# Kernel tuning notes

Hardware: AMD Instinct MI355X
Metric: run time of the kernel (lower is better)

The kernel has to match this reference:

```python
import jax, jax.numpy as jnp
import numpy as np

B, HH, WW, C, HEADS = 2, 128, 128, 256, 8
D = C // HEADS


def setup_inputs() -> dict:
    key = jax.random.key(0)
    ks = jax.random.split(key, 24)
    def nrm(k, shape, s=0.02):
        return jax.random.normal(k, shape, jnp.float32) * s
    inp = {
        'x_2': jax.random.normal(ks[0], (B, HH, WW, C), jnp.float32),
        'x_4': jax.random.normal(ks[1], (B, HH, WW, C), jnp.float32),
        'x_8': jax.random.normal(ks[2], (B, HH, WW, C), jnp.float32),
        'y':   jax.random.normal(ks[3], (B, HH, WW, C), jnp.float32),
        'Wqm': nrm(ks[4], (C, C)), 'Wkm': nrm(ks[5], (C, C)), 'Wvm': nrm(ks[6], (C, C)),
        'Wk2': nrm(ks[7], (C, C)), 'Wv2': nrm(ks[8], (C, C)),
        'Wk4': nrm(ks[9], (C, C)), 'Wv4': nrm(ks[10], (C, C)),
        'Wk8': nrm(ks[11], (C, C)), 'Wv8': nrm(ks[12], (C, C)),
        'rescalem': jnp.ones((HEADS, 1, 1), jnp.float32),
        'rescale2': jnp.ones((HEADS, 1, 1), jnp.float32),
        'rescale4': jnp.ones((HEADS, 1, 1), jnp.float32),
        'rescale8': jnp.ones((HEADS, 1, 1), jnp.float32),
        'Wproj': nrm(ks[13], (C, C)), 'bproj': jnp.zeros((C,), jnp.float32),
        'Wpos1': nrm(ks[14], (C, 1, 3, 3)), 'Wpos2': nrm(ks[15], (C, 1, 3, 3)),
    }
    return inp


def _l2norm(x):
    # F.normalize(p=2, dim=-1): x / max(||x||_2, eps)
    return x / jnp.maximum(jnp.linalg.norm(x, axis=-1, keepdims=True), 1e-12)


def _heads_T(t):
    # (b, n, h*d) -> (b, h, d, n)  (split heads then transpose last two dims)
    b, n, _ = t.shape
    return t.reshape(b, n, HEADS, D).transpose(0, 2, 3, 1)


def _dwconv(x, w):
    # x: NCHW, w: (C,1,3,3) depthwise
    return jax.lax.conv_general_dilated(
        x, w, (1, 1), 'SAME',
        dimension_numbers=('NCHW', 'OIHW', 'NCHW'),
        feature_group_count=C)


def reference(x_2, x_4, x_8, y,
              Wqm, Wkm, Wvm, Wk2, Wv2, Wk4, Wv4, Wk8, Wv8,
              rescalem, rescale2, rescale4, rescale8,
              Wproj, bproj, Wpos1, Wpos2):
    b, h, w, c = y.shape
    n = h * w
    x2 = x_2.reshape(b, n, c)
    x4 = x_4.reshape(b, n, c)
    x8 = x_8.reshape(b, n, c)
    yf = y.reshape(b, n, c)

    q_inpm = yf @ Wqm.T
    v_inpm = yf @ Wvm.T
    qm = _l2norm(_heads_T(q_inpm))  # (b,heads,d,n), L2-normalized over n

    def branch(k_inp, v_inp, rescale):
        k = _l2norm(_heads_T(k_inp))   # (b,heads,d,n)
        v = _heads_T(v_inp)            # (b,heads,d,n)
        attn = jnp.einsum('bhdn,bhen->bhde', k, qm) * rescale  # (b,heads,d,d)
        attn = jax.nn.softmax(attn, axis=-1)
        return jnp.einsum('bhde,bhen->bhdn', attn, v)

    # NOTE: original code uses rescale4 for the x8 branch (faithful to source).
    xo = (branch(yf @ Wkm.T, v_inpm, rescalem)
          + branch(x2 @ Wk2.T, x2 @ Wv2.T, rescale2)
          + branch(x4 @ Wk4.T, x4 @ Wv4.T, rescale4)
          + branch(x8 @ Wk8.T, x8 @ Wv8.T, rescale4))

    # (b,heads,d,n) -> (b,n,heads*d)
    xo = xo.transpose(0, 3, 1, 2).reshape(b, n, HEADS * D)
    out_c = (xo @ Wproj.T + bproj).reshape(b, h, w, c)

    p = v_inpm.reshape(b, h, w, c).transpose(0, 3, 1, 2)  # NCHW
    p = _dwconv(p, Wpos1)
    p = jax.nn.gelu(p, approximate=False)
    p = _dwconv(p, Wpos2)
    out_p = p.transpose(0, 2, 3, 1)

    return out_c + out_p
```

## Files before the change

kernel.cpp:

```cpp
#include <hip/hip_runtime.h>
#include <hip/hip_bf16.h>
#include <math.h>

typedef short bf16x8 __attribute__((ext_vector_type(8)));
typedef float f32x4 __attribute__((ext_vector_type(4)));

#define MFMA16(a,b,c) __builtin_amdgcn_mfma_f32_16x16x32_bf16(a,b,c,0,0,0)

__device__ inline short f2bf(float f){
  union{ __hip_bfloat16 h; short s; } u;
  u.h = __float2bfloat16(f);
  return u.s;
}
__device__ inline float bf2f(short s){
  uint32_t u = ((uint32_t)(uint16_t)s) << 16;
  return __builtin_bit_cast(float, u);
}
__device__ inline void store8bf(short* dst, float4 a, float4 b){
  union{ short s[8]; int4 q; } u;
  u.s[0]=f2bf(a.x); u.s[1]=f2bf(a.y); u.s[2]=f2bf(a.z); u.s[3]=f2bf(a.w);
  u.s[4]=f2bf(b.x); u.s[5]=f2bf(b.y); u.s[6]=f2bf(b.z); u.s[7]=f2bf(b.w);
  *(int4*)dst = u.q;
}

__device__ inline void gld16(const void* g, void* l){
  __builtin_amdgcn_global_load_lds(
      (const __attribute__((address_space(1))) unsigned int*)g,
      (__attribute__((address_space(3))) unsigned int*)l, 16, 0, 0);
}

#define BARC() do{ asm volatile("":::"memory"); __builtin_amdgcn_s_barrier(); \
                   asm volatile("":::"memory"); }while(0)

__global__ __launch_bounds__(256) void k_cvt(const float* __restrict__ src, short* __restrict__ dst, int n){
  int i = blockIdx.x*256 + threadIdx.x;
  if(i < n) dst[i] = f2bf(src[i]);
}

__global__ __launch_bounds__(256) void k_cvtN(const float* __restrict__ src, short* __restrict__ dst,
                                              int n, int ncpy){
  int i = blockIdx.x*256 + threadIdx.x;
  if(i >= n) return;
  float s = src[i];
  for(int c=1;c<ncpy;++c) s += src[i + (size_t)c*917504];
  dst[i] = f2bf(s);
}

__global__ __launch_bounds__(256) void k_wvt(const float* __restrict__ wm, const float* __restrict__ w2,
                                             const float* __restrict__ w4, const float* __restrict__ w8,
                                             short* __restrict__ wvT){
  int t = blockIdx.x*256 + threadIdx.x;
  int br = t >> 16; int rem = t & 65535; int a = rem >> 8, j = rem & 255;
  const float* w = (br==0)? wm : (br==1)? w2 : (br==2)? w4 : w8;
  wvT[t] = f2bf(w[j*256 + a]);
}

__global__ __launch_bounds__(256) void k_wT(const float* __restrict__ w1, const float* __restrict__ w2,
                                            float* __restrict__ wT){
  int t = blockIdx.x*256 + threadIdx.x;
  if(t >= 4608) return;
  int cv = t / 2304; int rem = t % 2304; int tap = rem >> 8; int c = rem & 255;
  const float* w = cv ? w2 : w1;
  wT[t] = w[c*9 + tap];
}

__global__ __launch_bounds__(256) void k_pack(const float* __restrict__ x2, const float* __restrict__ x4,
                                              const float* __restrict__ x8, const float* __restrict__ y,
                                              short* __restrict__ xt){
  int sb = blockIdx.z; int s = sb >> 1, b = sb & 1;
  const float* src = ((s==0)? y : (s==1)? x2 : (s==2)? x4 : x8) + (size_t)b*16384*256;
  __shared__ short tile[64*264];
  int t = threadIdx.x, l = t & 63, w = t >> 6;
  int n0 = blockIdx.x*64;
  #pragma unroll
  for(int p=0;p<16;++p){
    int row = p*4 + w;
    float4 v = *(const float4*)(src + (size_t)(n0+row)*256 + 4*l);
    union{ short s4[4]; int2 q; } u;
    u.s4[0]=f2bf(v.x); u.s4[1]=f2bf(v.y); u.s4[2]=f2bf(v.z); u.s4[3]=f2bf(v.w);
    *(int2*)&tile[row*264 + 4*l] = u.q;
  }
  __syncthreads();
  int c = t;
  short* outb = xt + ((size_t)sb*512 + (n0>>5))*8192;
  int sw = (c>>1)&3;
  #pragma unroll
  for(int ti=0; ti<2; ++ti){
    union{ short v[32]; int4 q4[4]; } rowv;
    #pragma unroll
    for(int j=0;j<32;++j) rowv.v[j] = tile[(ti*32+j)*264 + c];
    char* ob = (char*)(outb + (size_t)ti*8192 + c*32);
    #pragma unroll
    for(int hi=0;hi<4;++hi)
      *(int4*)(ob + ((hi ^ sw)<<4)) = rowv.q4[hi];
  }
}

__device__ inline bf16x8 tfrag(const short* base, int c, int hi){
  int byte = c*64 + ((hi ^ ((c>>1)&3))<<4);
  return *(const bf16x8*)((const char*)base + byte);
}

__global__ __launch_bounds__(512,2) void k_cov(const short* __restrict__ xt, float* __restrict__ covF,
                                               int plain){
  int jb = blockIdx.x;
  int ck = blockIdx.y;
  int j = jb >> 1, b = jb & 1;
  int t = threadIdx.x, l = t & 63, w = t >> 6;
  int lr = l & 15, hi = l >> 4;
  __shared__ short lds3[3][16384];
  int su = (j < 4) ? 0 : (j - 3);
  int sv = (j == 0) ? 0 : ((j < 4) ? j : (j - 3));
  int sym = (su == sv);
  const short* Ug = xt + (size_t)(su*2+b)*512*8192;
  const short* Vg = xt + (size_t)(sv*2+b)*512*8192;
  int nt0 = ck*32;

  f32x4 acc[2][16];
  #pragma unroll
  for(int i=0;i<2;++i)
    #pragma unroll
    for(int n2=0;n2<16;++n2) acc[i][n2] = (f32x4){0.f,0.f,0.f,0.f};

  #define STAGE_S(bufi, kk) do{                                                 \
    const short* Ut_ = Ug + (size_t)(nt0+(kk))*8192;                            \
    short* dst_ = &lds3[bufi][0];                                               \
    _Pragma("unroll")                                                           \
    for(int i_=0;i_<2;++i_){ int ch_ = w*2+i_;                                  \
      gld16(Ut_ + ch_*512 + l*8, dst_ + ch_*512); }                             \
  }while(0)
  #define STAGE_A(bufi, kk) do{                                                 \
    const short* Ut_ = Ug + (size_t)(nt0+(kk))*8192;                            \
    const short* Vt_ = Vg + (size_t)(nt0+(kk))*8192;                            \
    short* dst_ = &lds3[bufi][0];                                               \
    _Pragma("unroll")                                                           \
    for(int i_=0;i_<4;++i_){ int ch_ = w*4+i_;                                  \
      const short* g_ = (ch_<16) ? (Ut_ + ch_*512 + l*8)                        \
                                 : (Vt_ + (ch_-16)*512 + l*8);                  \
      gld16(g_, dst_ + ch_*512); }                                              \
  }while(0)
  #define COMPUTE(bufp, vofs) do{                                               \
    const short* Ub_ = bufp;                                                    \
    const short* Vb_ = Ub_ + (vofs);                                            \
    bf16x8 a0_ = tfrag(Ub_, w*32 + lr, hi);                                     \
    bf16x8 a1_ = tfrag(Ub_, w*32 + 16 + lr, hi);                                \
    _Pragma("unroll")                                                           \
    for(int nt_=0;nt_<16;++nt_){                                                \
      bf16x8 bb_ = tfrag(Vb_, nt_*16 + lr, hi);                                 \
      acc[0][nt_] = MFMA16(a0_, bb_, acc[0][nt_]);                              \
      acc[1][nt_] = MFMA16(a1_, bb_, acc[1][nt_]);                              \
    }                                                                           \
  }while(0)

  if(sym){
    STAGE_S(0,0); STAGE_S(1,1); STAGE_S(2,2);
    asm volatile("s_waitcnt vmcnt(4)":::"memory");
    BARC();
    int buf = 0;
    #pragma unroll 1
    for(int k=0;k<32;++k){
      COMPUTE(&lds3[buf][0], 0);
      if(k==31) break;
      BARC();
      if(k < 29){
        STAGE_S(buf, k+3);
        asm volatile("s_waitcnt vmcnt(4)":::"memory");
      } else if(k == 29){
        asm volatile("s_waitcnt vmcnt(2)":::"memory");
      } else {
        asm volatile("s_waitcnt vmcnt(0)":::"memory");
      }
      BARC();
      buf = (buf==2)?0:(buf+1);
    }
  } else {
    STAGE_A(0,0); STAGE_A(1,1); STAGE_A(2,2);
    asm volatile("s_waitcnt vmcnt(8)":::"memory");
    BARC();
    int buf = 0;
    #pragma unroll 1
    for(int k=0;k<32;++k){
      COMPUTE(&lds3[buf][0], 8192);
      if(k==31) break;
      BARC();
      if(k < 29){
        STAGE_A(buf, k+3);
        asm volatile("s_waitcnt vmcnt(8)":::"memory");
      } else if(k == 29){
        asm volatile("s_waitcnt vmcnt(4)":::"memory");
      } else {
        asm volatile("s_waitcnt vmcnt(0)":::"memory");
      }
      BARC();
      buf = (buf==2)?0:(buf+1);
    }
  }
  #undef STAGE_S
  #undef STAGE_A
  #undef COMPUTE

  if(plain){
    float* cov = covF + (size_t)ck*917504 + (size_t)jb*65536;
    #pragma unroll
    for(int rt=0;rt<2;++rt)
      #pragma unroll
      for(int nt=0;nt<16;++nt)
        #pragma unroll
        for(int r=0;r<4;++r){
          int row = w*32 + rt*16 + 4*hi + r;
          int col = nt*16 + lr;
          cov[(size_t)row*256 + col] = acc[rt][nt][r];
        }
  } else {
    float* cov = covF + (size_t)jb*65536;
    #pragma unroll
    for(int rt=0;rt<2;++rt)
      #pragma unroll
      for(int nt=0;nt<16;++nt)
        #pragma unroll
        for(int r=0;r<4;++r){
          int row = w*32 + rt*16 + 4*hi + r;
          int col = nt*16 + lr;
          atomicAdd(&cov[(size_t)row*256 + col], acc[rt][nt][r]);
        }
  }
}

__device__ inline void mm_32x256(const short (*wA)[264], const short* __restrict__ covbf,
                                 short (*tmp)[264], int t){
  int l = t & 63, w = t >> 6;
  int mt = w >> 1, ntb = (w & 1)*8;
  f32x4 acc[8];
  #pragma unroll
  for(int i=0;i<8;++i) acc[i] = (f32x4){0.f,0.f,0.f,0.f};
  #pragma unroll
  for(int kk=0; kk<8; ++kk){
    bf16x8 a = *(const bf16x8*)&wA[16*mt + (l&15)][kk*32 + 8*(l>>4)];
    #pragma unroll
    for(int n=0; n<8; ++n){
      int j = (ntb+n)*16 + (l&15);
      bf16x8 bb = *(const bf16x8*)&covbf[(size_t)j*256 + kk*32 + 8*(l>>4)];
      acc[n] = MFMA16(a, bb, acc[n]);
    }
  }
  #pragma unroll
  for(int n=0;n<8;++n)
    #pragma unroll
    for(int r=0;r<4;++r)
      tmp[16*mt + 4*(l>>4) + r][(ntb+n)*16 + (l&15)] = f2bf(acc[n][r]);
}
__device__ inline void mm_32x32(const short (*A)[264], const short (*Bw)[264], float (*M)[33], int t){
  int l = t & 63, w = t >> 6;
  int mt = w >> 1, nt = w & 1;
  f32x4 acc = (f32x4){0.f,0.f,0.f,0.f};
  #pragma unroll
  for(int kk=0; kk<8; ++kk){
    bf16x8 a = *(const bf16x8*)&A[16*mt + (l&15)][kk*32 + 8*(l>>4)];
    bf16x8 b = *(const bf16x8*)&Bw[16*nt + (l&15)][kk*32 + 8*(l>>4)];
    acc = MFMA16(a, b, acc);
  }
  #pragma unroll
  for(int r=0;r<4;++r)
    M[16*mt + 4*(l>>4) + r][16*nt + (l&15)] = acc[r];
}

__global__ __launch_bounds__(256) void k_attn(
    const float* __restrict__ Wq, const float* __restrict__ Wkm, const float* __restrict__ Wk2,
    const float* __restrict__ Wk4, const float* __restrict__ Wk8,
    const float* __restrict__ rsm, const float* __restrict__ rs2, const float* __restrict__ rs4,
    const short* __restrict__ covB, float* __restrict__ Aout){
  int h = blockIdx.x, b = blockIdx.y, br = blockIdx.z;
  int t = threadIdx.x;
  __shared__ short wk[32][264], wq[32][264], tmp[32][264];
  __shared__ float Ml[32][33];
  __shared__ float nrm[64];
  const float* Wk = (br==0)? Wkm : (br==1)? Wk2 : (br==2)? Wk4 : Wk8;
  {
    int d = t >> 3, c0 = (t & 7)*32;
    const float* pk = Wk + (size_t)(h*32+d)*256 + c0;
    const float* pq = Wq + (size_t)(h*32+d)*256 + c0;
    #pragma unroll
    for(int i=0;i<32;i+=8){
      float4 a1 = *(const float4*)(pk+i), a2 = *(const float4*)(pk+i+4);
      store8bf(&wk[d][c0+i], a1, a2);
      float4 b1 = *(const float4*)(pq+i), b2 = *(const float4*)(pq+i+4);
      store8bf(&wq[d][c0+i], b1, b2);
    }
  }
  __syncthreads();
  const short* cxy = covB + (size_t)(br*2+b)*65536;
  const short* cxx = (br==0)? cxy : covB + (size_t)(8 + (br-1)*2 + b)*65536;
  const short* cyy = covB + (size_t)b*65536;
  mm_32x256(wk, cxx, tmp, t); __syncthreads();
  mm_32x32(tmp, wk, Ml, t);   __syncthreads();
  if(t < 32) nrm[t] = Ml[t][t];
  __syncthreads();
  mm_32x256(wq, cyy, tmp, t); __syncthreads();
  mm_32x32(tmp, wq, Ml, t);   __syncthreads();
  if(t < 32) nrm[32+t] = Ml[t][t];
  __syncthreads();
  mm_32x256(wk, cxy, tmp, t); __syncthreads();
  mm_32x32(tmp, wq, Ml, t);   __syncthreads();
  if(t < 32){
    int d = t;
    const float* rs = (br==0)? rsm : (br==1)? rs2 : rs4;
    float rsv = rs[h];
    float invk = 1.f / fmaxf(sqrtf(fmaxf(nrm[d], 0.f)), 1e-12f);
    float lg[32]; float mx = -1e30f;
    #pragma unroll
    for(int e=0;e<32;++e){
      float invq = 1.f / fmaxf(sqrtf(fmaxf(nrm[32+e], 0.f)), 1e-12f);
      float v = Ml[d][e] * invk * invq * rsv;
      lg[e] = v; mx = fmaxf(mx, v);
    }
    float sum = 0.f;
    #pragma unroll
    for(int e=0;e<32;++e){ lg[e] = expf(lg[e]-mx); sum += lg[e]; }
    float inv = 1.f/sum;
    float* Ao = Aout + ((size_t)((br*2+b)*8 + h))*1024 + d*32;
    #pragma unroll
    for(int e=0;e<32;++e) Ao[e] = lg[e]*inv;
  }
}

__global__ __launch_bounds__(256) void k_qfold(const float* __restrict__ Wproj, const float* __restrict__ Ain,
                                               const short* __restrict__ wvT, short* __restrict__ qf){
  int cg = blockIdx.x, b = blockIdx.y, br = blockIdx.z;
  int t = threadIdx.x;
  __shared__ float Al[8*1036];
  __shared__ short pl[32][264];
  const float* Ag = Ain + (size_t)((br*2+b)*8)*1024;
  for(int i=t; i<8192; i+=256){
    int hh = i >> 10, dd = (i >> 5) & 31, ee = i & 31;
    Al[hh*1036 + dd*32 + ee] = Ag[i];
  }
  __syncthreads();
  {
    int c = cg*32 + (t >> 3), h = t & 7;
    const float* wpr = Wproj + (size_t)c*256 + h*32;
    float wp[32];
    #pragma unroll
    for(int i=0;i<32;i+=4){
      float4 v = *(const float4*)(wpr+i);
      wp[i]=v.x; wp[i+1]=v.y; wp[i+2]=v.z; wp[i+3]=v.w;
    }
    float pv[32];
    #pragma unroll
    for(int e=0;e<32;++e) pv[e]=0.f;
    const float* Ah = Al + h*1036;
    #pragma unroll
    for(int d=0; d<32; ++d){
      float wpd = wp[d];
      #pragma unroll
      for(int e=0;e<32;e+=4){
        float4 av = *(const float4*)&Ah[d*32+e];
        pv[e]   += wpd*av.x; pv[e+1] += wpd*av.y;
        pv[e+2] += wpd*av.z; pv[e+3] += wpd*av.w;
      }
    }
    #pragma unroll
    for(int e=0;e<32;++e) pl[t>>3][h*32+e] = f2bf(pv[e]);
  }
  __syncthreads();
  {
    int l = t & 63, w = t >> 6, mt = w >> 1, ntb = (w & 1)*8;
    const short* wvt = wvT + (size_t)br*65536;
    f32x4 acc[8];
    #pragma unroll
    for(int i=0;i<8;++i) acc[i] = (f32x4){0.f,0.f,0.f,0.f};
    #pragma unroll
    for(int kk=0; kk<8; ++kk){
      bf16x8 a = *(const bf16x8*)&pl[16*mt + (l&15)][kk*32 + 8*(l>>4)];
      #pragma unroll
      for(int n=0;n<8;++n){
        int arow = (ntb+n)*16 + (l&15);
        bf16x8 bb = *(const bf16x8*)&wvt[(size_t)arow*256 + kk*32 + 8*(l>>4)];
        acc[n] = MFMA16(a, bb, acc[n]);
      }
    }
    short* qfp = qf + (size_t)(br*2+b)*65536;
    #pragma unroll
    for(int n=0;n<8;++n)
      #pragma unroll
      for(int r=0;r<4;++r){
        int row = cg*32 + 16*mt + 4*(l>>4) + r;
        int col = (ntb+n)*16 + (l&15);
        qfp[(size_t)row*256 + col] = f2bf(acc[n][r]);
      }
  }
}

__device__ inline void at_write4(short* base, int row, int l, float4 v){
  union{ short s[4]; int2 q; } u;
  u.s[0]=f2bf(v.x); u.s[1]=f2bf(v.y); u.s[2]=f2bf(v.z); u.s[3]=f2bf(v.w);
  int byte = row*512 + 8*l;
  byte ^= ((row&7)<<4);
  *(int2*)((char*)base + byte) = u.q;
}
__device__ inline bf16x8 at_read8(const short* base, int row, int kk, int q){
  int byte = row*512 + kk*64 + q*16;
  byte ^= ((row&7)<<4);
  return *(const bf16x8*)((const char*)base + byte);
}

__global__ __launch_bounds__(256,2) void k_vm(const float* __restrict__ y, const short* __restrict__ wB,
                                              short* __restrict__ vm){
  int t = threadIdx.x, l = t & 63, w = t >> 6;
  size_t m0 = (size_t)blockIdx.x*64;
  __shared__ short at[64*256];
  #pragma unroll
  for(int rr=0; rr<16; ++rr){
    int row = w*16 + rr;
    float4 v = *(const float4*)(y + (m0+row)*256 + 4*l);
    at_write4(at, row, l, v);
  }
  __syncthreads();
  f32x4 acc[4][4];
  #pragma unroll
  for(int i=0;i<4;++i)
    #pragma unroll
    for(int n2=0;n2<4;++n2) acc[i][n2] = (f32x4){0.f,0.f,0.f,0.f};
  #pragma unroll
  for(int kk=0; kk<8; ++kk){
    bf16x8 a[4];
    #pragma unroll
    for(int rt=0;rt<4;++rt) a[rt] = at_read8(at, rt*16 + (l&15), kk, l>>4);
    #pragma unroll
    for(int nt=0;nt<4;++nt){
      int bc = (w*4+nt)*16 + (l&15);
      bf16x8 bb = *(const bf16x8*)&wB[(size_t)bc*256 + kk*32 + 8*(l>>4)];
      #pragma unroll
      for(int rt=0;rt<4;++rt) acc[rt][nt] = MFMA16(a[rt], bb, acc[rt][nt]);
    }
  }
  #pragma unroll
  for(int rt=0;rt<4;++rt)
    #pragma unroll
    for(int nt=0;nt<4;++nt)
      #pragma unroll
      for(int r=0;r<4;++r){
        size_t row = m0 + rt*16 + 4*(l>>4) + r;
        int col = (w*4+nt)*16 + (l&15);
        vm[row*256 + col] = f2bf(acc[rt][nt][r]);
      }
}

__global__ __launch_bounds__(256) void k_conv(const short* __restrict__ in, const float* __restrict__ wT,
                                              short* __restrict__ out, int do_gelu){
  int tid = blockIdx.x*256 + threadIdx.x;
  int cg = tid & 31; int pix = tid >> 5;
  int x = pix & 127, yy = (pix >> 7) & 127, b = pix >> 14;
  int c0 = cg*8;
  float acc[8];
  #pragma unroll
  for(int i=0;i<8;++i) acc[i]=0.f;
  #pragma unroll
  for(int ky=0; ky<3; ++ky){
    int sy = yy + ky - 1;
    if(sy < 0 || sy > 127) continue;
    #pragma unroll
    for(int kx=0; kx<3; ++kx){
      int sx = x + kx - 1;
      if(sx < 0 || sx > 127) continue;
      const float* wp = wT + (ky*3+kx)*256 + c0;
      float4 w0 = *(const float4*)wp;
      float4 w1 = *(const float4*)(wp+4);
      const short* p = in + ((size_t)(((b<<7)+sy)<<7) + sx)*256 + c0;
      union{ int4 q; short s[8]; } u;
      u.q = *(const int4*)p;
      acc[0] += bf2f(u.s[0])*w0.x; acc[1] += bf2f(u.s[1])*w0.y;
      acc[2] += bf2f(u.s[2])*w0.z; acc[3] += bf2f(u.s[3])*w0.w;
      acc[4] += bf2f(u.s[4])*w1.x; acc[5] += bf2f(u.s[5])*w1.y;
      acc[6] += bf2f(u.s[6])*w1.z; acc[7] += bf2f(u.s[7])*w1.w;
    }
  }
  if(do_gelu){
    #pragma unroll
    for(int cc=0;cc<8;++cc)
      acc[cc] = 0.5f*acc[cc]*(1.f + erff(acc[cc]*0.70710678118654752f));
  }
  union{ int4 q; short s[8]; } o;
  #pragma unroll
  for(int cc=0;cc<8;++cc) o.s[cc] = f2bf(acc[cc]);
  *(int4*)(out + (size_t)pix*256 + c0) = o.q;
}

__global__ __launch_bounds__(256,2) void k_final(const float* __restrict__ y, const float* __restrict__ x2,
                                                 const float* __restrict__ x4, const float* __restrict__ x8,
                                                 const short* __restrict__ qf, const float* __restrict__ bproj,
                                                 const short* __restrict__ pos, float* __restrict__ out){
  int t = threadIdx.x, l = t & 63, w = t >> 6;
  size_t m0 = (size_t)blockIdx.x*64;
  int b = (int)(m0 >> 14);
  __shared__ short at[64*256];
  f32x4 acc[4][4];
  #pragma unroll
  for(int i=0;i<4;++i)
    #pragma unroll
    for(int n2=0;n2<4;++n2) acc[i][n2] = (f32x4){0.f,0.f,0.f,0.f};
  const float* srcs[4] = {y, x2, x4, x8};
  #pragma unroll 1
  for(int br=0; br<4; ++br){
    __syncthreads();
    #pragma unroll
    for(int rr=0; rr<16; ++rr){
      int row = w*16 + rr;
      float4 v = *(const float4*)(srcs[br] + (m0+row)*256 + 4*l);
      at_write4(at, row, l, v);
    }
    __syncthreads();
    const short* qb = qf + (size_t)(br*2+b)*65536;
    #pragma unroll
    for(int kk=0; kk<8; ++kk){
      bf16x8 a[4];
      #pragma unroll
      for(int rt=0;rt<4;++rt) a[rt] = at_read8(at, rt*16 + (l&15), kk, l>>4);
      #pragma unroll
      for(int nt=0;nt<4;++nt){
        int bc = (w*4+nt)*16 + (l&15);
        bf16x8 bb = *(const bf16x8*)&qb[(size_t)bc*256 + kk*32 + 8*(l>>4)];
        #pragma unroll
        for(int rt=0;rt<4;++rt) acc[rt][nt] = MFMA16(a[rt], bb, acc[rt][nt]);
      }
    }
  }
  #pragma unroll
  for(int rt=0;rt<4;++rt)
    #pragma unroll
    for(int nt=0;nt<4;++nt)
      #pragma unroll
      for(int r=0;r<4;++r){
        size_t row = m0 + rt*16 + 4*(l>>4) + r;
        int col = (w*4+nt)*16 + (l&15);
        out[row*256 + col] = acc[rt][nt][r] + bproj[col] + bf2f(pos[row*256 + col]);
      }
}

extern "C" void kernel_launch(void* const* d_in, const int* in_sizes, int n_in,
                              void* d_out, int out_size, void* d_ws, size_t ws_size,
                              hipStream_t stream){
  (void)in_sizes; (void)n_in; (void)out_size;
  const float* x2   = (const float*)d_in[0];
  const float* x4   = (const float*)d_in[1];
  const float* x8   = (const float*)d_in[2];
  const float* y    = (const float*)d_in[3];
  const float* Wq   = (const float*)d_in[4];
  const float* Wkm  = (const float*)d_in[5];
  const float* Wvm  = (const float*)d_in[6];
  const float* Wk2  = (const float*)d_in[7];
  const float* Wv2  = (const float*)d_in[8];
  const float* Wk4  = (const float*)d_in[9];
  const float* Wv4  = (const float*)d_in[10];
  const float* Wk8  = (const float*)d_in[11];
  const float* Wv8  = (const float*)d_in[12];
  const float* rsm  = (const float*)d_in[13];
  const float* rs2  = (const float*)d_in[14];
  const float* rs4  = (const float*)d_in[15];
  const float* Wproj= (const float*)d_in[17];
  const float* bproj= (const float*)d_in[18];
  const float* Wp1  = (const float*)d_in[19];
  const float* Wp2  = (const float*)d_in[20];
  float* out = (float*)d_out;

  char* ws = (char*)d_ws;
  short* XT2  = (short*)(ws + 0);
  short* VM   = (short*)(ws + 0);
  short* GBUF = (short*)(ws + 16777216);
  short* POS  = (short*)(ws + 33554432);
  float* wT   = (float*)(ws + 50331648);

  const size_t NEED16 = 129630208;
  int plain = (ws_size >= NEED16) ? 1 : 0;

  float* covF; short* covB; float* Aout; short* QF; short* WvmB; short* WvT;
  if(plain){
    covF = (float*)(ws + 67108864);
    covB = (short*)(ws + 125829120);
    Aout = (float*)(ws + 127664128);
    QF   = (short*)(ws + 127926272);
    WvmB = (short*)(ws + 128974848);
    WvT  = (short*)(ws + 129105920);
  } else {
    covF = (float*)(ws + 67108864);
    covB = (short*)(ws + 70778880);
    Aout = (float*)(ws + 72613888);
    QF   = (short*)(ws + 72876032);
    WvmB = (short*)(ws + 73924608);
    WvT  = (short*)(ws + 74055680);
  }

  if(!plain) hipMemsetAsync(covF, 0, 3670016, stream);
  k_cvt  <<<256, 256, 0, stream>>>(Wvm, WvmB, 65536);
  k_wvt  <<<1024, 256, 0, stream>>>(Wvm, Wv2, Wv4, Wv8, WvT);
  k_pack <<<dim3(256,1,8), 256, 0, stream>>>(x2, x4, x8, y, XT2);
  k_cov  <<<dim3(14,16), 512, 0, stream>>>(XT2, covF, plain);
  k_cvtN <<<3584, 256, 0, stream>>>(covF, covB, 917504, plain ? 16 : 1);
  k_wT   <<<18, 256, 0, stream>>>(Wp1, Wp2, wT);
  k_attn <<<dim3(8,2,4), 256, 0, stream>>>(Wq, Wkm, Wk2, Wk4, Wk8, rsm, rs2, rs4, covB, Aout);
  k_qfold<<<dim3(8,2,4), 256, 0, stream>>>(Wproj, Aout, WvT, QF);
  k_vm   <<<512, 256, 0, stream>>>(y, WvmB, VM);
  k_conv <<<4096, 256, 0, stream>>>(VM, wT, GBUF, 1);
  k_conv <<<4096, 256, 0, stream>>>(GBUF, wT + 2304, POS, 0);
  k_final<<<512, 256, 0, stream>>>(y, x2, x4, x8, QF, bproj, POS, out);
}
```

Before: 261.9 us.

## Double-buffer cov K-tiles in pairs and prefetch next branch input in k_final

The covariance kernel moves from a 3-slot single-tile ring to two buffers of two K-tiles each. Each barrier interval now covers two tiles of MFMA work, halving barrier count, but LDS per block doubles and the occupancy hint of 2 is dropped. The final projection kernel double-buffers its LDS A tile and loads the next branch's fp32 rows into registers while the current branch computes, overlapping global loads with MFMA at the cost of 64 extra VGPRs per thread.

```diff
diff --git a/kernel.cpp b/kernel.cpp
--- a/kernel.cpp
+++ b/kernel.cpp
@@ -101,14 +101,14 @@
   return *(const bf16x8*)((const char*)base + byte);
 }
 
-__global__ __launch_bounds__(512,2) void k_cov(const short* __restrict__ xt, float* __restrict__ covF,
-                                               int plain){
+__global__ __launch_bounds__(512) void k_cov(const short* __restrict__ xt, float* __restrict__ covF,
+                                             int plain){
   int jb = blockIdx.x;
   int ck = blockIdx.y;
   int j = jb >> 1, b = jb & 1;
   int t = threadIdx.x, l = t & 63, w = t >> 6;
   int lr = l & 15, hi = l >> 4;
-  __shared__ short lds3[3][16384];
+  __shared__ short lds2[2][32768];
   int su = (j < 4) ? 0 : (j - 3);
   int sv = (j == 0) ? 0 : ((j < 4) ? j : (j - 3));
   int sym = (su == sv);
@@ -122,24 +122,24 @@
     #pragma unroll
     for(int n2=0;n2<16;++n2) acc[i][n2] = (f32x4){0.f,0.f,0.f,0.f};
 
-  #define STAGE_S(bufi, kk) do{                                                 \
+  #define STAGE_T_S(bufi, tt, kk) do{                                           \
     const short* Ut_ = Ug + (size_t)(nt0+(kk))*8192;                            \
-    short* dst_ = &lds3[bufi][0];                                               \
+    short* dst_ = &lds2[bufi][(tt)*16384];                                      \
     _Pragma("unroll")                                                           \
     for(int i_=0;i_<2;++i_){ int ch_ = w*2+i_;                                  \
       gld16(Ut_ + ch_*512 + l*8, dst_ + ch_*512); }                             \
   }while(0)
-  #define STAGE_A(bufi, kk) do{                                                 \
+  #define STAGE_T_A(bufi, tt, kk) do{                                           \
     const short* Ut_ = Ug + (size_t)(nt0+(kk))*8192;                            \
     const short* Vt_ = Vg + (size_t)(nt0+(kk))*8192;                            \
-    short* dst_ = &lds3[bufi][0];                                               \
+    short* dst_ = &lds2[bufi][(tt)*16384];                                      \
     _Pragma("unroll")                                                           \
     for(int i_=0;i_<4;++i_){ int ch_ = w*4+i_;                                  \
       const short* g_ = (ch_<16) ? (Ut_ + ch_*512 + l*8)                        \
                                  : (Vt_ + (ch_-16)*512 + l*8);                  \
       gld16(g_, dst_ + ch_*512); }                                              \
   }while(0)
-  #define COMPUTE(bufp, vofs) do{                                               \
+  #define COMPUTE_T(bufp, vofs) do{                                             \
     const short* Ub_ = bufp;                                                    \
     const short* Vb_ = Ub_ + (vofs);                                            \
     bf16x8 a0_ = tfrag(Ub_, w*32 + lr, hi);                                     \
@@ -153,51 +153,47 @@
   }while(0)
 
   if(sym){
-    STAGE_S(0,0); STAGE_S(1,1); STAGE_S(2,2);
+    STAGE_T_S(0,0,0); STAGE_T_S(0,1,1); STAGE_T_S(1,0,2); STAGE_T_S(1,1,3);
     asm volatile("s_waitcnt vmcnt(4)":::"memory");
     BARC();
-    int buf = 0;
     #pragma unroll 1
-    for(int k=0;k<32;++k){
-      COMPUTE(&lds3[buf][0], 0);
-      if(k==31) break;
+    for(int p=0;p<16;++p){
+      const short* base = &lds2[p&1][0];
+      COMPUTE_T(base, 0);
+      COMPUTE_T(base + 16384, 0);
+      if(p==15) break;
       BARC();
-      if(k < 29){
-        STAGE_S(buf, k+3);
-        asm volatile("s_waitcnt vmcnt(4)":::"memory");
-      } else if(k == 29){
-        asm volatile("s_waitcnt vmcnt(2)":::"memory");
-      } else {
-        asm volatile("s_waitcnt vmcnt(0)":::"memory");
-      }
-      BARC();
-      buf = (buf==2)?0:(buf+1);
-    }
-  } else {
-    STAGE_A(0,0); STAGE_A(1,1); STAGE_A(2,2);
-    asm volatile("s_waitcnt vmcnt(8)":::"memory");
-    BARC();
-    int buf = 0;
-    #pragma unroll 1
-    for(int k=0;k<32;++k){
-      COMPUTE(&lds3[buf][0], 8192);
-      if(k==31) break;
-      BARC();
-      if(k < 29){
-        STAGE_A(buf, k+3);
-        asm volatile("s_waitcnt vmcnt(8)":::"memory");
-      } else if(k == 29){
+      if(p < 14){
+        STAGE_T_S(p&1, 0, 2*p+4); STAGE_T_S(p&1, 1, 2*p+5);
         asm volatile("s_waitcnt vmcnt(4)":::"memory");
       } else {
         asm volatile("s_waitcnt vmcnt(0)":::"memory");
       }
       BARC();
-      buf = (buf==2)?0:(buf+1);
-    }
-  }
-  #undef STAGE_S
-  #undef STAGE_A
-  #undef COMPUTE
+    }
+  } else {
+    STAGE_T_A(0,0,0); STAGE_T_A(0,1,1); STAGE_T_A(1,0,2); STAGE_T_A(1,1,3);
+    asm volatile("s_waitcnt vmcnt(8)":::"memory");
+    BARC();
+    #pragma unroll 1
+    for(int p=0;p<16;++p){
+      const short* base = &lds2[p&1][0];
+      COMPUTE_T(base, 8192);
+      COMPUTE_T(base + 16384, 8192);
+      if(p==15) break;
+      BARC();
+      if(p < 14){
+        STAGE_T_A(p&1, 0, 2*p+4); STAGE_T_A(p&1, 1, 2*p+5);
+        asm volatile("s_waitcnt vmcnt(8)":::"memory");
+      } else {
+        asm volatile("s_waitcnt vmcnt(0)":::"memory");
+      }
+      BARC();
+    }
+  }
+  #undef STAGE_T_S
+  #undef STAGE_T_A
+  #undef COMPUTE_T
 
   if(plain){
     float* cov = covF + (size_t)ck*917504 + (size_t)jb*65536;
@@ -492,29 +488,37 @@
   int t = threadIdx.x, l = t & 63, w = t >> 6;
   size_t m0 = (size_t)blockIdx.x*64;
   int b = (int)(m0 >> 14);
-  __shared__ short at[64*256];
+  __shared__ short at2[2][64*256];
   f32x4 acc[4][4];
   #pragma unroll
   for(int i=0;i<4;++i)
     #pragma unroll
     for(int n2=0;n2<4;++n2) acc[i][n2] = (f32x4){0.f,0.f,0.f,0.f};
   const float* srcs[4] = {y, x2, x4, x8};
+  float4 vreg[16];
+  #pragma unroll
+  for(int rr=0; rr<16; ++rr)
+    vreg[rr] = *(const float4*)(srcs[0] + (m0 + w*16 + rr)*256 + 4*l);
   #pragma unroll 1
   for(int br=0; br<4; ++br){
-    __syncthreads();
-    #pragma unroll
-    for(int rr=0; rr<16; ++rr){
-      int row = w*16 + rr;
-      float4 v = *(const float4*)(srcs[br] + (m0+row)*256 + 4*l);
-      at_write4(at, row, l, v);
-    }
-    __syncthreads();
+    short* buf = &at2[br&1][0];
+    #pragma unroll
+    for(int rr=0; rr<16; ++rr)
+      at_write4(buf, w*16 + rr, l, vreg[rr]);
+    if(br < 3){
+      const float* s = srcs[br+1];
+      #pragma unroll
+      for(int rr=0; rr<16; ++rr)
+        vreg[rr] = *(const float4*)(s + (m0 + w*16 + rr)*256 + 4*l);
+    }
+    asm volatile("s_waitcnt lgkmcnt(0)":::"memory");
+    BARC();
     const short* qb = qf + (size_t)(br*2+b)*65536;
     #pragma unroll
     for(int kk=0; kk<8; ++kk){
       bf16x8 a[4];
       #pragma unroll
-      for(int rt=0;rt<4;++rt) a[rt] = at_read8(at, rt*16 + (l&15), kk, l>>4);
+      for(int rt=0;rt<4;++rt) a[rt] = at_read8(buf, rt*16 + (l&15), kk, l>>4);
       #pragma unroll
       for(int nt=0;nt<4;++nt){
         int bc = (w*4+nt)*16 + (l&15);
```

After: 253.3 us. 1.03x faster.
